# Kernel optimization log

Hardware: AMD Instinct MI355X
Metric: run time of the kernel (lower is better)

The kernel has to match this reference:

```python
import jax, jax.numpy as jnp
import numpy as np

VOCAB = 100000; E = 256; H = 256; Hh = 128; K = 12
START = 9; STOP = 10; PAD = 11; NEG = -10000.0
B = 32; T = 512


def setup_inputs() -> dict:
    key = jax.random.key(0)
    ks = jax.random.split(key, 16)
    u = 1.0 / np.sqrt(Hh)  # pytorch LSTM init scale
    xav = lambda k, shape: jax.random.normal(k, shape, jnp.float32) * np.sqrt(2.0 / (shape[0] + shape[1]))
    trans = jax.random.normal(ks[10], (K, K), jnp.float32)
    trans = trans.at[START, :].set(NEG).at[:, STOP].set(NEG)
    trans = trans.at[PAD, :].set(NEG).at[:, PAD].set(NEG)
    return {
        "sentence": jax.random.randint(ks[0], (B, T), 0, VOCAB),
        "h0": jax.random.normal(ks[1], (2, B, Hh), jnp.float32),
        "c0": jax.random.normal(ks[2], (2, B, Hh), jnp.float32),
        "embed": xav(ks[3], (VOCAB, E)),
        "W_ih_f": jax.random.uniform(ks[4], (4 * Hh, E), jnp.float32, -u, u),
        "W_hh_f": jax.random.uniform(ks[5], (4 * Hh, Hh), jnp.float32, -u, u),
        "b_f": jax.random.uniform(ks[6], (4 * Hh,), jnp.float32, -u, u),
        "W_ih_r": jax.random.uniform(ks[7], (4 * Hh, E), jnp.float32, -u, u),
        "W_hh_r": jax.random.uniform(ks[8], (4 * Hh, Hh), jnp.float32, -u, u),
        "b_r": jax.random.uniform(ks[9], (4 * Hh,), jnp.float32, -u, u),
        "W_out": xav(ks[11], (K, H)),
        "b_out": jnp.zeros((K,), jnp.float32),
        "transitions": trans,
    }


def _lstm_dir(xe, W_ih, W_hh, b, h0, c0):
    # xe: [T,B,E]; precompute input contribution once (big GEMM outside scan)
    xg = jnp.einsum('tbe,ge->tbg', xe, W_ih) + b  # [T,B,4*Hh]
    def step(carry, xt):
        h, c = carry
        g = xt + h @ W_hh.T
        i, f, gg, o = jnp.split(g, 4, axis=-1)  # pytorch gate order i,f,g,o
        c = jax.nn.sigmoid(f) * c + jax.nn.sigmoid(i) * jnp.tanh(gg)
        h = jax.nn.sigmoid(o) * jnp.tanh(c)
        return (h, c), h
    _, hs = jax.lax.scan(step, (h0, c0), xg)
    return hs  # [T,B,Hh]


def reference(sentence, h0, c0, embed, W_ih_f, W_hh_f, b_f, W_ih_r, W_hh_r, b_r,
              W_out, b_out, transitions):
    xe = embed[sentence].transpose(1, 0, 2)  # [T,B,E]
    hs_f = _lstm_dir(xe, W_ih_f, W_hh_f, b_f, h0[0], c0[0])
    hs_r = _lstm_dir(xe[::-1], W_ih_r, W_hh_r, b_r, h0[1], c0[1])[::-1]
    hs = jnp.concatenate([hs_f, hs_r], axis=-1)           # [T,B,H]
    feats = hs @ W_out.T + b_out                          # [T,B,K]

    # Viterbi max-plus recurrence
    scores0 = jnp.full((B, K), NEG, jnp.float32).at[:, START].set(0.0)
    def vstep(scores, feat):
        m = scores[:, None, :] + transitions[None, :, :]  # [B,K_next,K_prev]
        ptr = jnp.argmax(m, axis=-1).astype(jnp.int32)
        return jnp.max(m, axis=-1) + feat, ptr
    scores, pointers = jax.lax.scan(vstep, scores0, feats)  # pointers [T,B,K]
    scores = scores + transitions[STOP]
    best_tag = jnp.argmax(scores, axis=-1).astype(jnp.int32)  # [B]

    # parallel backtrace (reverse scan, outputs in original time order)
    def back(tag, ptr):
        prev = jnp.take_along_axis(ptr, tag[:, None], axis=1)[:, 0]
        return prev, tag
    _, path = jax.lax.scan(back, best_tag, pointers, reverse=True)  # [T,B]
    return path.T  # [B,T] int32 best tag sequence
```

## Files before the change

### kernel.cpp

```cpp
#include <hip/hip_runtime.h>
#include <hip/hip_bf16.h>
#include <cmath>

#define TT 512
#define BB 32
#define EE 256
#define HH 128
#define KCRF 12
#define NEGF (-10000.0f)

__global__ __launch_bounds__(256) void k1_xg(const int* __restrict__ sent,
    const float* __restrict__ embed,
    const float* __restrict__ Wf, const float* __restrict__ bf,
    const float* __restrict__ Wr, const float* __restrict__ br,
    float* __restrict__ XG)
{
  __shared__ __align__(16) float As[64][36];
  __shared__ __align__(16) float Bs[128][36];
  const int tid = threadIdx.x;
  const int m0 = (blockIdx.x >> 3) * 64;
  const int n0 = (blockIdx.x & 7) * 128;
  const int ty = tid >> 4, tx = tid & 15;
  float acc[4][8];
#pragma unroll
  for (int i = 0; i < 4; ++i)
#pragma unroll
    for (int j = 0; j < 8; ++j) acc[i][j] = 0.f;

  for (int k0 = 0; k0 < 256; k0 += 32) {
#pragma unroll
    for (int r = 0; r < 2; ++r) {
      int idx = tid + r * 256;
      int row = idx >> 3;
      int c4 = (idx & 7) << 2;
      int R = m0 + row;
      int t = R >> 5, b = R & 31;
      const float4 v = *(const float4*)(embed + (long)sent[b * TT + t] * 256 + k0 + c4);
      *(float4*)&As[row][c4] = v;
    }
#pragma unroll
    for (int r = 0; r < 4; ++r) {
      int idx = tid + r * 256;
      int row = idx >> 3;
      int c4 = (idx & 7) << 2;
      int col = n0 + row;
      const float* src = (col < 512) ? (Wf + (long)col * 256) : (Wr + (long)(col - 512) * 256);
      const float4 v = *(const float4*)(src + k0 + c4);
      *(float4*)&Bs[row][c4] = v;
    }
    __syncthreads();
#pragma unroll
    for (int kk = 0; kk < 32; ++kk) {
      float a[4], bv[8];
#pragma unroll
      for (int i = 0; i < 4; ++i) a[i] = As[ty * 4 + i][kk];
#pragma unroll
      for (int j = 0; j < 8; ++j) bv[j] = Bs[tx + 16 * j][kk];
#pragma unroll
      for (int i = 0; i < 4; ++i)
#pragma unroll
        for (int j = 0; j < 8; ++j) acc[i][j] = fmaf(a[i], bv[j], acc[i][j]);
    }
    __syncthreads();
  }
#pragma unroll
  for (int i = 0; i < 4; ++i) {
    int R = m0 + ty * 4 + i;
#pragma unroll
    for (int j = 0; j < 8; ++j) {
      int col = n0 + tx + 16 * j;
      float bias = (col < 512) ? bf[col] : br[col - 512];
      XG[(long)R * 1024 + col] = acc[i][j] + bias;
    }
  }
}

__global__ __launch_bounds__(512) void k2_scan(const float* __restrict__ XG,
    const float* __restrict__ Whf, const float* __restrict__ Whr,
    const float* __restrict__ h0, const float* __restrict__ c0,
    float* __restrict__ HS)
{
  const int wg = blockIdx.x;
  const int dir = wg >> 5;
  const int b = wg & 31;
  const int j = threadIdx.x;
  const float* Wh = dir ? Whr : Whf;

  float w[128];
#pragma unroll
  for (int i = 0; i < 32; ++i) {
    float4 v = *(const float4*)(Wh + (long)j * 128 + i * 4);
    w[4 * i + 0] = v.x; w[4 * i + 1] = v.y; w[4 * i + 2] = v.z; w[4 * i + 3] = v.w;
  }

  __shared__ __align__(16) float hs[128];
  __shared__ float gs[512];
  float c = 0.f;
  if (j < 128) {
    hs[j] = h0[(dir * 32 + b) * 128 + j];
    c = c0[(dir * 32 + b) * 128 + j];
  }
  __syncthreads();

  const int t0 = dir ? (TT - 1) : 0;
  float xg_cur = XG[((long)t0 * 32 + b) * 1024 + dir * 512 + j];
  const int gate = j >> 7;

  for (int s = 0; s < TT; ++s) {
    const int t = dir ? (TT - 1 - s) : s;
    float xg_nxt = 0.f;
    if (s + 1 < TT) {
      int tn = dir ? (TT - 2 - s) : (s + 1);
      xg_nxt = XG[((long)tn * 32 + b) * 1024 + dir * 512 + j];
    }
    float acc = xg_cur;
#pragma unroll
    for (int i = 0; i < 32; ++i) {
      float4 hv = *(const float4*)(hs + 4 * i);
      acc = fmaf(w[4 * i + 0], hv.x, acc);
      acc = fmaf(w[4 * i + 1], hv.y, acc);
      acc = fmaf(w[4 * i + 2], hv.z, acc);
      acc = fmaf(w[4 * i + 3], hv.w, acc);
    }
    float act = (gate == 2) ? tanhf(acc) : (1.f / (1.f + expf(-acc)));
    gs[j] = act;
    __syncthreads();
    if (j < 128) {
      float ig = gs[j], fg = gs[128 + j], gg = gs[256 + j], og = gs[384 + j];
      c = fmaf(fg, c, ig * gg);
      float h = og * tanhf(c);
      hs[j] = h;
      HS[((long)t * 32 + b) * 256 + dir * 128 + j] = h;
    }
    __syncthreads();
    xg_cur = xg_nxt;
  }
}

__global__ __launch_bounds__(64) void k3_feats(const float* __restrict__ HS,
    const float* __restrict__ Wout, const float* __restrict__ bout,
    float* __restrict__ FE)
{
  __shared__ __align__(16) float ws[12 * 256];
  __shared__ float bs[12];
  const int tid = threadIdx.x;
  for (int i = tid; i < 768; i += 64)
    ((float4*)ws)[i] = ((const float4*)Wout)[i];
  if (tid < 12) bs[tid] = bout[tid];
  __syncthreads();
  const long row = (long)blockIdx.x * 64 + tid;
  const float4* hp = (const float4*)(HS + row * 256);
  float acc[12];
#pragma unroll
  for (int k = 0; k < 12; ++k) acc[k] = bs[k];
  for (int e4 = 0; e4 < 64; ++e4) {
    float4 hv = hp[e4];
#pragma unroll
    for (int k = 0; k < 12; ++k) {
      const float4 wv = *(const float4*)&ws[k * 256 + e4 * 4];
      acc[k] = fmaf(hv.x, wv.x, acc[k]);
      acc[k] = fmaf(hv.y, wv.y, acc[k]);
      acc[k] = fmaf(hv.z, wv.z, acc[k]);
      acc[k] = fmaf(hv.w, wv.w, acc[k]);
    }
  }
  const int t = (int)(row >> 5), b = (int)(row & 31);
#pragma unroll
  for (int k = 0; k < 12; ++k) FE[((long)t * 12 + k) * 32 + b] = acc[k];
}

__global__ __launch_bounds__(384) void k4_viterbi(const float* __restrict__ FE,
    const float* __restrict__ trans, unsigned char* __restrict__ PTR,
    int* __restrict__ out)
{
  __shared__ float sc[32][13];
  __shared__ float tr[144];
  __shared__ int btag[32];
  const int tid = threadIdx.x;
  const int b = tid & 31, nxt = tid >> 5;
  if (tid < 144) tr[tid] = trans[tid];
  if (nxt == 0) {
#pragma unroll
    for (int p = 0; p < 12; ++p) sc[b][p] = (p == 9) ? 0.f : NEGF;
  }
  __syncthreads();
  float fnext = FE[nxt * 32 + b];
  for (int t = 0; t < TT; ++t) {
    const float feat = fnext;
    if (t + 1 < TT) fnext = FE[(t + 1) * 384 + nxt * 32 + b];
    float best = -1e30f; int arg = 0;
#pragma unroll
    for (int p = 0; p < 12; ++p) {
      float v = sc[b][p] + tr[nxt * 12 + p];
      if (v > best) { best = v; arg = p; }
    }
    __syncthreads();
    sc[b][nxt] = best + feat;
    PTR[(t * 32 + b) * 12 + nxt] = (unsigned char)arg;
    __syncthreads();
  }
  if (nxt == 0) {
    float best = -1e30f; int arg = 0;
#pragma unroll
    for (int p = 0; p < 12; ++p) {
      float v = sc[b][p] + tr[10 * 12 + p];
      if (v > best) { best = v; arg = p; }
    }
    btag[b] = arg;
  }
  __syncthreads();
  if (tid < 32) {
    int tag = btag[b];
    for (int t = TT - 1; t >= 0; --t) {
      out[b * TT + t] = tag;
      if (t > 0) tag = PTR[(t * 32 + b) * 12 + tag];
    }
  }
}

extern "C" void kernel_launch(void* const* d_in, const int* in_sizes, int n_in,
                              void* d_out, int out_size, void* d_ws, size_t ws_size,
                              hipStream_t stream)
{
  const int* sent = (const int*)d_in[0];
  const float* h0 = (const float*)d_in[1];
  const float* c0 = (const float*)d_in[2];
  const float* embed = (const float*)d_in[3];
  const float* Wif = (const float*)d_in[4];
  const float* Whf = (const float*)d_in[5];
  const float* bf = (const float*)d_in[6];
  const float* Wir = (const float*)d_in[7];
  const float* Whr = (const float*)d_in[8];
  const float* br = (const float*)d_in[9];
  const float* Wout = (const float*)d_in[10];
  const float* bout = (const float*)d_in[11];
  const float* trans = (const float*)d_in[12];

  char* ws = (char*)d_ws;
  float* XG = (float*)ws;
  float* HS = (float*)(ws + 67108864);
  float* FE = (float*)(ws + 67108864 + 16777216);
  unsigned char* PTR = (unsigned char*)(ws + 67108864 + 16777216 + 786432);
  int* out = (int*)d_out;

  hipLaunchKernelGGL(k1_xg, dim3(2048), dim3(256), 0, stream,
                     sent, embed, Wif, bf, Wir, br, XG);
  hipLaunchKernelGGL(k2_scan, dim3(64), dim3(512), 0, stream,
                     XG, Whf, Whr, h0, c0, HS);
  hipLaunchKernelGGL(k3_feats, dim3(256), dim3(64), 0, stream,
                     HS, Wout, bout, FE);
  hipLaunchKernelGGL(k4_viterbi, dim3(1), dim3(384), 0, stream,
                     FE, trans, PTR, out);
}
```

Baseline: 931.5 us.

## Broadcast LSTM hidden state via readlane and keep Viterbi pointers in LDS

In the recurrent LSTM scan, each lane now loads two hidden values and the 128-wide matvec gets the rest by scalar readlane broadcasts, using four independent accumulators. This replaces repeated float4 LDS reads of the whole hidden vector on every step, and the launch bounds now request two waves per execution unit. The single-block Viterbi kernel double-buffers its score array to drop one barrier per step. It also packs backpointers as 4-bit nibbles in shared memory instead of writing bytes to global memory and reading them back during the backtrace. This costs about 98 KB of LDS and adds extra packing work per step.

```diff
diff --git a/kernel.cpp b/kernel.cpp
--- a/kernel.cpp
+++ b/kernel.cpp
@@ -8,6 +8,8 @@
 #define HH 128
 #define KCRF 12
 #define NEGF (-10000.0f)
+
+#define RL(v, l) __uint_as_float(__builtin_amdgcn_readlane(__float_as_uint(v), (l)))
 
 __global__ __launch_bounds__(256) void k1_xg(const int* __restrict__ sent,
     const float* __restrict__ embed,
@@ -75,7 +77,7 @@
   }
 }
 
-__global__ __launch_bounds__(512) void k2_scan(const float* __restrict__ XG,
+__global__ __launch_bounds__(512, 2) void k2_scan(const float* __restrict__ XG,
     const float* __restrict__ Whf, const float* __restrict__ Whr,
     const float* __restrict__ h0, const float* __restrict__ c0,
     float* __restrict__ HS)
@@ -84,6 +86,7 @@
   const int dir = wg >> 5;
   const int b = wg & 31;
   const int j = threadIdx.x;
+  const int lane = j & 63;
   const float* Wh = dir ? Whr : Whf;
 
   float w[128];
@@ -113,16 +116,22 @@
       int tn = dir ? (TT - 2 - s) : (s + 1);
       xg_nxt = XG[((long)tn * 32 + b) * 1024 + dir * 512 + j];
     }
-    float acc = xg_cur;
-#pragma unroll
-    for (int i = 0; i < 32; ++i) {
-      float4 hv = *(const float4*)(hs + 4 * i);
-      acc = fmaf(w[4 * i + 0], hv.x, acc);
-      acc = fmaf(w[4 * i + 1], hv.y, acc);
-      acc = fmaf(w[4 * i + 2], hv.z, acc);
-      acc = fmaf(w[4 * i + 3], hv.w, acc);
-    }
-    float act = (gate == 2) ? tanhf(acc) : (1.f / (1.f + expf(-acc)));
+    const float2 hp = *(const float2*)(hs + 2 * lane);
+    float a0 = xg_cur, a1 = 0.f, a2 = 0.f, a3 = 0.f;
+#pragma unroll
+    for (int l = 0; l < 64; ++l) {
+      const float sh0 = RL(hp.x, l);
+      const float sh1 = RL(hp.y, l);
+      if (l & 1) {
+        a2 = fmaf(sh0, w[2 * l + 0], a2);
+        a3 = fmaf(sh1, w[2 * l + 1], a3);
+      } else {
+        a0 = fmaf(sh0, w[2 * l + 0], a0);
+        a1 = fmaf(sh1, w[2 * l + 1], a1);
+      }
+    }
+    const float acc = (a0 + a1) + (a2 + a3);
+    const float act = (gate == 2) ? tanhf(acc) : (1.f / (1.f + expf(-acc)));
     gs[j] = act;
     __syncthreads();
     if (j < 128) {
@@ -170,40 +179,52 @@
 }
 
 __global__ __launch_bounds__(384) void k4_viterbi(const float* __restrict__ FE,
-    const float* __restrict__ trans, unsigned char* __restrict__ PTR,
-    int* __restrict__ out)
-{
-  __shared__ float sc[32][13];
+    const float* __restrict__ trans, int* __restrict__ out)
+{
+  __shared__ unsigned char nib[TT * 192];
+  __shared__ float sc[2][32][12];
   __shared__ float tr[144];
+  __shared__ unsigned char stag[2][384];
   __shared__ int btag[32];
   const int tid = threadIdx.x;
   const int b = tid & 31, nxt = tid >> 5;
   if (tid < 144) tr[tid] = trans[tid];
   if (nxt == 0) {
 #pragma unroll
-    for (int p = 0; p < 12; ++p) sc[b][p] = (p == 9) ? 0.f : NEGF;
+    for (int p = 0; p < 12; ++p) sc[0][b][p] = (p == 9) ? 0.f : NEGF;
   }
   __syncthreads();
   float fnext = FE[nxt * 32 + b];
   for (int t = 0; t < TT; ++t) {
+    const int cur = t & 1;
     const float feat = fnext;
     if (t + 1 < TT) fnext = FE[(t + 1) * 384 + nxt * 32 + b];
     float best = -1e30f; int arg = 0;
 #pragma unroll
     for (int p = 0; p < 12; ++p) {
-      float v = sc[b][p] + tr[nxt * 12 + p];
+      float v = sc[cur][b][p] + tr[nxt * 12 + p];
       if (v > best) { best = v; arg = p; }
     }
-    __syncthreads();
-    sc[b][nxt] = best + feat;
-    PTR[(t * 32 + b) * 12 + nxt] = (unsigned char)arg;
-    __syncthreads();
+    sc[cur ^ 1][b][nxt] = best + feat;
+    stag[cur][b * 12 + nxt] = (unsigned char)arg;
+    if (t > 0 && tid < 192) {
+      const int bb = tid / 6, p = tid % 6;
+      nib[(t - 1) * 192 + tid] =
+          (unsigned char)(stag[cur ^ 1][bb * 12 + 2 * p] |
+                          (stag[cur ^ 1][bb * 12 + 2 * p + 1] << 4));
+    }
+    __syncthreads();
+  }
+  if (tid < 192) {
+    const int bb = tid / 6, p = tid % 6;
+    nib[511 * 192 + tid] =
+        (unsigned char)(stag[1][bb * 12 + 2 * p] | (stag[1][bb * 12 + 2 * p + 1] << 4));
   }
   if (nxt == 0) {
     float best = -1e30f; int arg = 0;
 #pragma unroll
     for (int p = 0; p < 12; ++p) {
-      float v = sc[b][p] + tr[10 * 12 + p];
+      float v = sc[0][b][p] + tr[10 * 12 + p];
       if (v > best) { best = v; arg = p; }
     }
     btag[b] = arg;
@@ -213,7 +234,10 @@
     int tag = btag[b];
     for (int t = TT - 1; t >= 0; --t) {
       out[b * TT + t] = tag;
-      if (t > 0) tag = PTR[(t * 32 + b) * 12 + tag];
+      if (t) {
+        unsigned char v = nib[t * 192 + b * 6 + (tag >> 1)];
+        tag = (tag & 1) ? (v >> 4) : (v & 15);
+      }
     }
   }
 }
@@ -240,7 +264,6 @@
   float* XG = (float*)ws;
   float* HS = (float*)(ws + 67108864);
   float* FE = (float*)(ws + 67108864 + 16777216);
-  unsigned char* PTR = (unsigned char*)(ws + 67108864 + 16777216 + 786432);
   int* out = (int*)d_out;
 
   hipLaunchKernelGGL(k1_xg, dim3(2048), dim3(256), 0, stream,
@@ -250,5 +273,5 @@
   hipLaunchKernelGGL(k3_feats, dim3(256), dim3(64), 0, stream,
                      HS, Wout, bout, FE);
   hipLaunchKernelGGL(k4_viterbi, dim3(1), dim3(384), 0, stream,
-                     FE, trans, PTR, out);
-}
+                     FE, trans, out);
+}
```

After: 986.6 us. +5.9%, slower.
